# Performance work log

Measured on AMD Instinct MI355X. Metric: run time of the kernel, lower is better.

Reference implementation:

```python
import jax, jax.numpy as jnp
import numpy as np

D = 64          # embed_dim == latent dim
T = 200         # diffusion_steps, timestep_respacing='' -> full 200 reverse steps
B, L = 8192, 100
N_ITEMS = 100000


def setup_inputs() -> dict:
    key = jax.random.key(0)
    ks = jax.random.split(key, 16)

    def lin(k, i, o):
        return (jax.random.normal(k, (i, o), jnp.float32) / np.sqrt(i)).astype(jnp.float32)

    item_seq = jax.random.randint(ks[0], (B, L), 0, N_ITEMS)
    item_emb = jax.random.normal(ks[1], (N_ITEMS, D), jnp.float32) * 0.02
    item_emb = item_emb.at[0].set(0.0)  # padding_idx=0
    return {
        'item_seq': item_seq,
        'item_emb': item_emb,
        'W_enc1': lin(ks[2], D, 256), 'b_enc1': jnp.zeros((256,), jnp.float32),
        'W_enc2': lin(ks[3], 256, 2 * D), 'b_enc2': jnp.zeros((2 * D,), jnp.float32),
        'W_in': lin(ks[4], D, D), 'b_in': jnp.zeros((D,), jnp.float32),
        'W_t': lin(ks[5], D, D), 'b_t': jnp.zeros((D,), jnp.float32),
        'W_c': lin(ks[6], D, D), 'b_c': jnp.zeros((D,), jnp.float32),
        'W_out': lin(ks[7], D, D), 'b_out': jnp.zeros((D,), jnp.float32),
    }


def _schedule():
    # improved-diffusion linear schedule
    scale = 1000.0 / T
    betas = jnp.linspace(scale * 1e-4, scale * 0.02, T, dtype=jnp.float32)
    alphas = 1.0 - betas
    acp = jnp.cumprod(alphas)
    acp_prev = jnp.concatenate([jnp.ones((1,), jnp.float32), acp[:-1]])
    sqrt_recip = jnp.sqrt(1.0 / acp)
    sqrt_recipm1 = jnp.sqrt(1.0 / acp - 1.0)
    post_var = betas * (1.0 - acp_prev) / (1.0 - acp)
    post_logvar = jnp.log(jnp.concatenate([post_var[1:2], post_var[1:]]))  # clipped
    coef1 = betas * jnp.sqrt(acp_prev) / (1.0 - acp)
    coef2 = (1.0 - acp_prev) * jnp.sqrt(alphas) / (1.0 - acp)
    return sqrt_recip, sqrt_recipm1, post_logvar, coef1, coef2


def reference(item_seq, item_emb, W_enc1, b_enc1, W_enc2, b_enc2,
              W_in, b_in, W_t, b_t, W_c, b_c, W_out, b_out):
    # ---- pooled VAE encoder (eval mode: dropout = identity, z = mu) ----
    seq = item_emb[item_seq]                                   # [B, L, D] gather
    cnt = jnp.sum(item_seq != 0, axis=1, keepdims=True).astype(seq.dtype)
    pooled = jnp.sum(seq, axis=1) / jnp.sqrt(cnt)              # [B, D]
    h = jax.nn.relu(pooled @ W_enc1 + b_enc1)
    enc = h @ W_enc2 + b_enc2                                  # [B, 2D]
    mu, logvar = jnp.split(enc, 2, axis=-1)
    z = mu                                                     # eval reparameterize

    # ---- ScoreNet: eps-prediction MLP conditioned on x_start and sinusoidal t ----
    half = D // 2
    freqs = jnp.exp(-jnp.log(10000.0) * jnp.arange(half, dtype=jnp.float32) / half)

    def scorenet(x, t_float, cond):
        ang = t_float * freqs                                  # [D/2]
        temb = jnp.concatenate([jnp.cos(ang), jnp.sin(ang)])   # [D]
        hh = jax.nn.silu(x @ W_in + b_in + (temb @ W_t + b_t) + cond @ W_c + b_c)
        return hh @ W_out + b_out                              # eps, [B, D]

    # ---- p_sample_loop (FIXED_SMALL variance, clip_denoised=True) ----
    sqrt_recip, sqrt_recipm1, post_logvar, coef1, coef2 = _schedule()
    x_init = jax.random.normal(jax.random.key(1), z.shape, z.dtype)
    noise_key = jax.random.key(2)

    def step(x, t):
        eps = scorenet(x, t.astype(jnp.float32), z)
        x0 = jnp.clip(sqrt_recip[t] * x - sqrt_recipm1[t] * eps, -1.0, 1.0)
        mean = coef1[t] * x0 + coef2[t] * x
        noise = jax.random.normal(jax.random.fold_in(noise_key, t), x.shape, x.dtype)
        sigma = jnp.where(t > 0, jnp.exp(0.5 * post_logvar[t]), 0.0)
        return mean + sigma * noise, None

    sample, _ = jax.lax.scan(step, x_init, jnp.arange(T - 1, -1, -1))
    return sample
```

## Files before the change

### kernel.cpp

```cpp
#include <hip/hip_runtime.h>
#include <cstdint>


#define DEVI __device__ __forceinline__

typedef __attribute__((ext_vector_type(8))) short short8;
typedef __attribute__((ext_vector_type(4))) float f32x4;

DEVI void threefry2x32(uint32_t k0, uint32_t k1, uint32_t x0, uint32_t x1,
                       uint32_t &o0, uint32_t &o1)
{
  const uint32_t ks2 = k0 ^ k1 ^ 0x1BD11BDAu;
  x0 += k0; x1 += k1;
#define TFR(r) { x0 += x1; x1 = __builtin_rotateleft32(x1, r); x1 ^= x0; }
  TFR(13u) TFR(15u) TFR(26u) TFR(6u)   x0 += k1;  x1 += ks2 + 1u;
  TFR(17u) TFR(29u) TFR(16u) TFR(24u)  x0 += ks2; x1 += k0 + 2u;
  TFR(13u) TFR(15u) TFR(26u) TFR(6u)   x0 += k0;  x1 += k1 + 3u;
  TFR(17u) TFR(29u) TFR(16u) TFR(24u)  x0 += k1;  x1 += ks2 + 4u;
  TFR(13u) TFR(15u) TFR(26u) TFR(6u)   x0 += ks2; x1 += k0 + 5u;
#undef TFR
  o0 = x0; o1 = x1;
}

DEVI uint32_t jax_random_bits32(uint32_t k0, uint32_t k1, uint32_t j)
{
  uint32_t a, b;
  threefry2x32(k0, k1, 0u, j, a, b);
  return a ^ b;
}

DEVI float jax_bits_to_normal(uint32_t bits)
{
  const float LO = -0.99999994f;
  float f = __uint_as_float((bits >> 9) | 0x3f800000u) - 1.0f;
  float u = fmaxf(LO, f * 2.0f + LO);
  float w = -__logf((1.0f - u) * (1.0f + u));
  float p;
  if (w < 5.0f) {
    w = w - 2.5f;
    p =              2.81022636e-08f;
    p = fmaf(p, w,   3.43273939e-07f);
    p = fmaf(p, w,  -3.5233877e-06f);
    p = fmaf(p, w,  -4.39150654e-06f);
    p = fmaf(p, w,   0.00021858087f);
    p = fmaf(p, w,  -0.00125372503f);
    p = fmaf(p, w,  -0.00417768164f);
    p = fmaf(p, w,   0.246640727f);
    p = fmaf(p, w,   1.50140941f);
  } else {
    w = sqrtf(w) - 3.0f;
    p =             -0.000200214257f;
    p = fmaf(p, w,   0.000100950558f);
    p = fmaf(p, w,   0.00134934322f);
    p = fmaf(p, w,  -0.00367342844f);
    p = fmaf(p, w,   0.00573950773f);
    p = fmaf(p, w,  -0.0076224613f);
    p = fmaf(p, w,   0.00943887047f);
    p = fmaf(p, w,   1.00167406f);
    p = fmaf(p, w,   2.83297682f);
  }
  return 1.41421356237f * (p * u);
}

DEVI short bf16_hi_trunc(float x) { return (short)(__float_as_uint(x) >> 16); }
DEVI float bf16_to_f32(short h)
{
  return __uint_as_float(((uint32_t)(unsigned short)h) << 16);
}
DEVI void split_bf16(float x, short &h, short &l)
{
  h = bf16_hi_trunc(x);
  float r = x - bf16_to_f32(h);
  l = bf16_hi_trunc(r);
}

DEVI short8 ld_frag16(const short* p)
{
  union { int4 v; short8 s; } u;
  u.v = *(const int4*)p;
  return u.s;
}

__global__ __launch_bounds__(64)
void k_prep(const float* __restrict__ Wt, const float* __restrict__ bt,
            const float* __restrict__ bin, float* __restrict__ tpb,
            float* __restrict__ sched)
{
  __shared__ float temb[64];
  const int t = blockIdx.x;
  const int d = threadIdx.x;
  const float lg = logf(10000.0f);
  {
    int i = d & 31;
    float fr  = expf((-lg * (float)i) / 32.0f);
    float ang = (float)t * fr;
    temb[d] = (d < 32) ? cosf(ang) : sinf(ang);
  }
  if (d == 0) {
    const float start = (float)(5.0 * 1e-4);
    const float stop  = (float)(5.0 * 0.02);
    const float delta = stop - start;
    float prod = 1.f, acp_prev = 1.f, beta = 0.f, alpha = 1.f;
    for (int i = 0; i <= t; ++i) {
      beta  = start + ((float)i * delta) / 199.0f;
      alpha = 1.0f - beta;
      acp_prev = prod;
      prod = prod * alpha;
    }
    float acp = prod;
    float om  = 1.0f - acp;
    sched[t * 8 + 0] = sqrtf(1.0f / acp);
    sched[t * 8 + 1] = sqrtf(1.0f / acp - 1.0f);
    sched[t * 8 + 2] = beta * sqrtf(acp_prev) / om;
    sched[t * 8 + 3] = (1.0f - acp_prev) * sqrtf(alpha) / om;
    float pv = beta * (1.0f - acp_prev) / om;
    sched[t * 8 + 4] = (t > 0) ? sqrtf(pv) : 0.0f;
    uint32_t fk0, fk1;
    threefry2x32(0u, 2u, 0u, (uint32_t)t, fk0, fk1);
    ((uint32_t*)sched)[t * 8 + 5] = fk0;
    ((uint32_t*)sched)[t * 8 + 6] = fk1;
  }
  __syncthreads();
  float acc = bt[d] + bin[d];
  for (int k = 0; k < 64; ++k)
    acc = fmaf(temb[k], Wt[k * 64 + d], acc);
  tpb[t * 64 + d] = acc;
}

#define XLDW  72
#define NBW   68

__global__
__attribute__((amdgpu_flat_work_group_size(512, 512), amdgpu_waves_per_eu(4, 4)))
void k_ddpm(const int* __restrict__ seq, const float* __restrict__ emb,
            const float* __restrict__ W1, const float* __restrict__ b1,
            const float* __restrict__ W2, const float* __restrict__ b2,
            const float* __restrict__ Wc, const float* __restrict__ bc,
            const float* __restrict__ Win, const float* __restrict__ Wout,
            const float* __restrict__ bout,
            const float* __restrict__ tpb, const float* __restrict__ sched,
            float* __restrict__ out)
{
  __shared__ __align__(16) char smem[28672];

  const int tid  = threadIdx.x;
  const int lane = tid & 63;
  const int w    = tid >> 6;
  const bool gemv = (w < 4);
  const int r0g  = blockIdx.x * 16;
  const uint32_t* su = (const uint32_t*)sched;

  const int nt   = w & 3;
  const int nn   = lane & 15;
  const int quad = lane >> 4;
  const int dim  = nt * 16 + nn;
  const int arow = nn;
  const int kq0  = quad * 8;
  const int kq1  = 32 + quad * 8;
  const int rowb = quad * 4;

  const int cb   = w * 128 + lane * 2;
  const uint32_t jn = (uint32_t)(r0g * 64 + cb);
  const int nrow = cb >> 6;
  const int ndim = cb & 63;

  {
    float* pool_s = (float*)smem;
    float* h_s    = (float*)(smem + 4096);
    float* mu_s   = (float*)(smem + 20480);
    float* cp_s   = (float*)(smem + 24576);

#pragma unroll
    for (int i = 0; i < 2; ++i) {
      int c = tid + i * 512;
      int row = c >> 6, d = c & 63;
      const int* rowp = seq + (r0g + row) * 100;
      float s = 0.f; int cnt = 0;
      for (int l = 0; l < 100; ++l) {
        int id = rowp[l];
        cnt += (id != 0);
        s += emb[id * 64 + d];
      }
      pool_s[row * 64 + d] = s / sqrtf((float)cnt);
    }
    __syncthreads();

#pragma unroll
    for (int i = 0; i < 8; ++i) {
      int c = tid + i * 512;
      int row = c >> 8, j = c & 255;
      float a = b1[j];
      for (int k = 0; k < 64; ++k)
        a = fmaf(pool_s[row * 64 + k], W1[k * 256 + j], a);
      h_s[row * 256 + j] = fmaxf(a, 0.f);
    }
    __syncthreads();

#pragma unroll
    for (int i = 0; i < 2; ++i) {
      int c = tid + i * 512;
      int row = c >> 6, j = c & 63;
      float a = b2[j];
      for (int k = 0; k < 256; ++k)
        a = fmaf(h_s[row * 256 + k], W2[k * 128 + j], a);
      mu_s[row * 64 + j] = a;
    }
    __syncthreads();

#pragma unroll
    for (int i = 0; i < 2; ++i) {
      int c = tid + i * 512;
      int row = c >> 6, j = c & 63;
      float a = bc[j];
      for (int k = 0; k < 64; ++k)
        a = fmaf(mu_s[row * 64 + k], Wc[k * 64 + j], a);
      cp_s[row * 64 + j] = a;
    }
    __syncthreads();
  }

  float cp[4] = {0.f, 0.f, 0.f, 0.f};
  if (gemv) {
    const float* cp_s = (const float*)(smem + 24576);
#pragma unroll
    for (int r = 0; r < 4; ++r) cp[r] = cp_s[(rowb + r) * 64 + dim];
  }
  __syncthreads();

  short* Xh = (short*)smem;
  short* Xl = (short*)(smem + 2304);
  short* Hh = (short*)(smem + 4608);
  short* Hl = (short*)(smem + 6912);
  float* nbuf = (float*)(smem + 9216);
  float* nb_w = &nbuf[nrow * NBW + ndim];

  short8 wiH0, wiL0, wiH1, wiL1, woH0, woL0, woH1, woL1;
  float xo[4] = {0.f, 0.f, 0.f, 0.f};
  float bo = 0.f, tp = 0.f;
  uint32_t j0 = 0;

  if (gemv) {
#pragma unroll
    for (int j = 0; j < 8; ++j) {
      short h, l;
      split_bf16(Win[(kq0 + j) * 64 + dim], h, l);  wiH0[j] = h; wiL0[j] = l;
      split_bf16(Win[(kq1 + j) * 64 + dim], h, l);  wiH1[j] = h; wiL1[j] = l;
      split_bf16(Wout[(kq0 + j) * 64 + dim], h, l); woH0[j] = h; woL0[j] = l;
      split_bf16(Wout[(kq1 + j) * 64 + dim], h, l); woH1[j] = h; woL1[j] = l;
    }
    bo = bout[dim];
    j0 = (uint32_t)((r0g + rowb) * 64 + dim);
#pragma unroll
    for (int r = 0; r < 4; ++r) {
      xo[r] = jax_bits_to_normal(jax_random_bits32(0u, 1u, j0 + r * 64u));
      short h, l;
      split_bf16(xo[r], h, l);
      Xh[(rowb + r) * XLDW + dim] = h; Xl[(rowb + r) * XLDW + dim] = l;
    }
    tp = tpb[199 * 64 + dim];
  }
  {
    const uint32_t fk0 = su[199 * 8 + 5];
    const uint32_t fk1 = su[199 * 8 + 6];
    float* d = nb_w + 16 * NBW;
    d[0] = jax_bits_to_normal(jax_random_bits32(fk0, fk1, jn + 0u));
    d[1] = jax_bits_to_normal(jax_random_bits32(fk0, fk1, jn + 1u));
  }
  __syncthreads();

#pragma unroll 1
  for (int t = 199; t >= 0; --t) {
    uint32_t gk0 = 0, gk1 = 0;
    float* nd = nullptr;
    if (t > 0) {
      gk0 = su[(t - 1) * 8 + 5];
      gk1 = su[(t - 1) * 8 + 6];
      nd = nb_w + ((t - 1) & 1) * 16 * NBW;
    }

    float sr = 0.f, srm1 = 0.f, c1 = 0.f, c2 = 0.f, sg = 0.f, tpn = 0.f;
    f32x4 acc;

    if (gemv) {
      sr   = sched[t * 8 + 0];
      srm1 = sched[t * 8 + 1];
      c1   = sched[t * 8 + 2];
      c2   = sched[t * 8 + 3];
      sg   = sched[t * 8 + 4];

#pragma unroll
      for (int r = 0; r < 4; ++r) acc[r] = tp + cp[r];
      {
        short8 xh0 = ld_frag16(&Xh[arow * XLDW + kq0]);
        short8 xl0 = ld_frag16(&Xl[arow * XLDW + kq0]);
        short8 xh1 = ld_frag16(&Xh[arow * XLDW + kq1]);
        short8 xl1 = ld_frag16(&Xl[arow * XLDW + kq1]);
        acc = __builtin_amdgcn_mfma_f32_16x16x32_bf16(xl0, wiH0, acc, 0, 0, 0);
        acc = __builtin_amdgcn_mfma_f32_16x16x32_bf16(xh0, wiL0, acc, 0, 0, 0);
        acc = __builtin_amdgcn_mfma_f32_16x16x32_bf16(xh0, wiH0, acc, 0, 0, 0);
        acc = __builtin_amdgcn_mfma_f32_16x16x32_bf16(xl1, wiH1, acc, 0, 0, 0);
        acc = __builtin_amdgcn_mfma_f32_16x16x32_bf16(xh1, wiL1, acc, 0, 0, 0);
        acc = __builtin_amdgcn_mfma_f32_16x16x32_bf16(xh1, wiH1, acc, 0, 0, 0);
      }
#pragma unroll
      for (int r = 0; r < 4; ++r) {
        float v = acc[r];
        v = v * __builtin_amdgcn_rcpf(1.0f + __expf(-v));
        short h, l;
        split_bf16(v, h, l);
        Hh[(rowb + r) * XLDW + dim] = h; Hl[(rowb + r) * XLDW + dim] = l;
      }
      int tn = (t > 0) ? (t - 1) : 0;
      tpn = tpb[tn * 64 + dim];
    }
    uint32_t b0 = 0, b1v = 0;
    if (t > 0) {
      b0  = jax_random_bits32(gk0, gk1, jn + 0u);
      b1v = jax_random_bits32(gk0, gk1, jn + 1u);
    }
    __syncthreads();

    if (gemv) {
      float n[4];
      const float* nr = &nbuf[(t & 1) * 16 * NBW + rowb * NBW + dim];
#pragma unroll
      for (int r = 0; r < 4; ++r) n[r] = nr[r * NBW];

      f32x4 eac;
#pragma unroll
      for (int r = 0; r < 4; ++r) eac[r] = bo;
      {
        short8 hh0 = ld_frag16(&Hh[arow * XLDW + kq0]);
        short8 hl0 = ld_frag16(&Hl[arow * XLDW + kq0]);
        short8 hh1 = ld_frag16(&Hh[arow * XLDW + kq1]);
        short8 hl1 = ld_frag16(&Hl[arow * XLDW + kq1]);
        eac = __builtin_amdgcn_mfma_f32_16x16x32_bf16(hl0, woH0, eac, 0, 0, 0);
        eac = __builtin_amdgcn_mfma_f32_16x16x32_bf16(hh0, woL0, eac, 0, 0, 0);
        eac = __builtin_amdgcn_mfma_f32_16x16x32_bf16(hh0, woH0, eac, 0, 0, 0);
        eac = __builtin_amdgcn_mfma_f32_16x16x32_bf16(hl1, woH1, eac, 0, 0, 0);
        eac = __builtin_amdgcn_mfma_f32_16x16x32_bf16(hh1, woL1, eac, 0, 0, 0);
        eac = __builtin_amdgcn_mfma_f32_16x16x32_bf16(hh1, woH1, eac, 0, 0, 0);
      }
#pragma unroll
      for (int r = 0; r < 4; ++r) {
        float xc = fminf(1.f, fmaxf(-1.f, sr * xo[r] - srm1 * eac[r]));
        xo[r] = c1 * xc + c2 * xo[r] + sg * n[r];
        short h, l;
        split_bf16(xo[r], h, l);
        Xh[(rowb + r) * XLDW + dim] = h; Xl[(rowb + r) * XLDW + dim] = l;
      }
      tp = tpn;
    }
    if (t > 0) {
      nd[0] = jax_bits_to_normal(b0);
      nd[1] = jax_bits_to_normal(b1v);
    }
    __syncthreads();
  }

  if (gemv) {
#pragma unroll
    for (int r = 0; r < 4; ++r) out[j0 + r * 64u] = xo[r];
  }
}

extern "C" void kernel_launch(void* const* d_in, const int* in_sizes, int n_in,
                              void* d_out, int out_size, void* d_ws, size_t ws_size,
                              hipStream_t stream)
{
  const int*   seq  = (const int*)  d_in[0];
  const float* emb  = (const float*)d_in[1];
  const float* W1   = (const float*)d_in[2];
  const float* b1   = (const float*)d_in[3];
  const float* W2   = (const float*)d_in[4];
  const float* b2   = (const float*)d_in[5];
  const float* Win  = (const float*)d_in[6];
  const float* bin  = (const float*)d_in[7];
  const float* Wt   = (const float*)d_in[8];
  const float* bt   = (const float*)d_in[9];
  const float* Wc   = (const float*)d_in[10];
  const float* bc   = (const float*)d_in[11];
  const float* Wout = (const float*)d_in[12];
  const float* bout = (const float*)d_in[13];

  float* out   = (float*)d_out;
  float* ws    = (float*)d_ws;
  float* tpb   = ws;
  float* sched = ws + 12800;

  k_prep <<<200, 64, 0, stream>>>(Wt, bt, bin, tpb, sched);
  k_ddpm <<<512, 512, 0, stream>>>(seq, emb, W1, b1, W2, b2, Wc, bc,
                                   Win, Wout, bout, tpb, sched, out);
}
```

Measured before the change: 560.8 us.

## Split pooling encoder into separate high-parallelism kernel merged with schedule prep

Moves the embedding gather, pooling, encoder MLP and condition projection out of the 512-block diffusion kernel into a new kernel with 1024 blocks of 256 threads, which also handles the per-timestep schedule and time-embedding work in 200 extra blocks. The condition projection goes to a workspace buffer that the diffusion kernel reads back per thread. The aim is to spread the memory-bound gather across more blocks and occupancy than the 512-thread kernel with its fixed waves-per-EU allowed, and to shrink that kernel's shared memory. The cost is a round trip through global memory for the projected condition.

Result: faster. 547.8 us (-2.3%).

```diff
diff --git a/kernel.cpp b/kernel.cpp
--- a/kernel.cpp
+++ b/kernel.cpp
@@ -81,50 +81,113 @@
   return u.s;
 }
 
-__global__ __launch_bounds__(64)
-void k_prep(const float* __restrict__ Wt, const float* __restrict__ bt,
-            const float* __restrict__ bin, float* __restrict__ tpb,
-            float* __restrict__ sched)
-{
-  __shared__ float temb[64];
-  const int t = blockIdx.x;
-  const int d = threadIdx.x;
-  const float lg = logf(10000.0f);
-  {
-    int i = d & 31;
-    float fr  = expf((-lg * (float)i) / 32.0f);
-    float ang = (float)t * fr;
-    temb[d] = (d < 32) ? cosf(ang) : sinf(ang);
-  }
-  if (d == 0) {
-    const float start = (float)(5.0 * 1e-4);
-    const float stop  = (float)(5.0 * 0.02);
-    const float delta = stop - start;
-    float prod = 1.f, acp_prev = 1.f, beta = 0.f, alpha = 1.f;
-    for (int i = 0; i <= t; ++i) {
-      beta  = start + ((float)i * delta) / 199.0f;
-      alpha = 1.0f - beta;
-      acp_prev = prod;
-      prod = prod * alpha;
-    }
-    float acp = prod;
-    float om  = 1.0f - acp;
-    sched[t * 8 + 0] = sqrtf(1.0f / acp);
-    sched[t * 8 + 1] = sqrtf(1.0f / acp - 1.0f);
-    sched[t * 8 + 2] = beta * sqrtf(acp_prev) / om;
-    sched[t * 8 + 3] = (1.0f - acp_prev) * sqrtf(alpha) / om;
-    float pv = beta * (1.0f - acp_prev) / om;
-    sched[t * 8 + 4] = (t > 0) ? sqrtf(pv) : 0.0f;
-    uint32_t fk0, fk1;
-    threefry2x32(0u, 2u, 0u, (uint32_t)t, fk0, fk1);
-    ((uint32_t*)sched)[t * 8 + 5] = fk0;
-    ((uint32_t*)sched)[t * 8 + 6] = fk1;
-  }
-  __syncthreads();
-  float acc = bt[d] + bin[d];
-  for (int k = 0; k < 64; ++k)
-    acc = fmaf(temb[k], Wt[k * 64 + d], acc);
-  tpb[t * 64 + d] = acc;
+__global__ __launch_bounds__(256)
+void k_poolenc(const int* __restrict__ seq, const float* __restrict__ emb,
+               const float* __restrict__ W1, const float* __restrict__ b1,
+               const float* __restrict__ W2, const float* __restrict__ b2,
+               const float* __restrict__ Wc, const float* __restrict__ bc,
+               float* __restrict__ cproj,
+               const float* __restrict__ Wt, const float* __restrict__ bt,
+               const float* __restrict__ bin, float* __restrict__ tpb,
+               float* __restrict__ sched)
+{
+  __shared__ float p_s[8 * 64];
+  __shared__ float h_s[8 * 256];
+  __shared__ float mu_s[8 * 64];
+  const int tid = threadIdx.x;
+
+  if (blockIdx.x < 1024u) {
+    const int r0 = blockIdx.x * 8;
+
+#pragma unroll
+    for (int i = 0; i < 2; ++i) {
+      int c = tid + i * 256;
+      int row = c >> 6, d = c & 63;
+      const int* rowp = seq + (r0 + row) * 100;
+      float s = 0.f; int cnt = 0;
+      for (int l = 0; l < 100; ++l) {
+        int id = rowp[l];
+        cnt += (id != 0);
+        s += emb[id * 64 + d];
+      }
+      p_s[row * 64 + d] = s / sqrtf((float)cnt);
+    }
+    __syncthreads();
+
+#pragma unroll
+    for (int i = 0; i < 8; ++i) {
+      int c = tid + i * 256;
+      int row = c >> 8, j = c & 255;
+      float a = b1[j];
+      for (int k = 0; k < 64; ++k)
+        a = fmaf(p_s[row * 64 + k], W1[k * 256 + j], a);
+      h_s[row * 256 + j] = fmaxf(a, 0.f);
+    }
+    __syncthreads();
+
+#pragma unroll
+    for (int i = 0; i < 2; ++i) {
+      int c = tid + i * 256;
+      int row = c >> 6, j = c & 63;
+      float a = b2[j];
+      for (int k = 0; k < 256; ++k)
+        a = fmaf(h_s[row * 256 + k], W2[k * 128 + j], a);
+      mu_s[row * 64 + j] = a;
+    }
+    __syncthreads();
+
+#pragma unroll
+    for (int i = 0; i < 2; ++i) {
+      int c = tid + i * 256;
+      int row = c >> 6, j = c & 63;
+      float a = bc[j];
+      for (int k = 0; k < 64; ++k)
+        a = fmaf(mu_s[row * 64 + k], Wc[k * 64 + j], a);
+      cproj[(r0 + row) * 64 + j] = a;
+    }
+  } else {
+    __shared__ float temb[64];
+    const int t = blockIdx.x - 1024;
+    const int d = tid;
+    if (d < 64) {
+      const float lg = logf(10000.0f);
+      int i = d & 31;
+      float fr  = expf((-lg * (float)i) / 32.0f);
+      float ang = (float)t * fr;
+      temb[d] = (d < 32) ? cosf(ang) : sinf(ang);
+      if (d == 0) {
+        const float start = (float)(5.0 * 1e-4);
+        const float stop  = (float)(5.0 * 0.02);
+        const float delta = stop - start;
+        float prod = 1.f, acp_prev = 1.f, beta = 0.f, alpha = 1.f;
+        for (int i2 = 0; i2 <= t; ++i2) {
+          beta  = start + ((float)i2 * delta) / 199.0f;
+          alpha = 1.0f - beta;
+          acp_prev = prod;
+          prod = prod * alpha;
+        }
+        float acp = prod;
+        float om  = 1.0f - acp;
+        sched[t * 8 + 0] = sqrtf(1.0f / acp);
+        sched[t * 8 + 1] = sqrtf(1.0f / acp - 1.0f);
+        sched[t * 8 + 2] = beta * sqrtf(acp_prev) / om;
+        sched[t * 8 + 3] = (1.0f - acp_prev) * sqrtf(alpha) / om;
+        float pv = beta * (1.0f - acp_prev) / om;
+        sched[t * 8 + 4] = (t > 0) ? sqrtf(pv) : 0.0f;
+        uint32_t fk0, fk1;
+        threefry2x32(0u, 2u, 0u, (uint32_t)t, fk0, fk1);
+        ((uint32_t*)sched)[t * 8 + 5] = fk0;
+        ((uint32_t*)sched)[t * 8 + 6] = fk1;
+      }
+    }
+    __syncthreads();
+    if (d < 64) {
+      float acc = bt[d] + bin[d];
+      for (int k = 0; k < 64; ++k)
+        acc = fmaf(temb[k], Wt[k * 64 + d], acc);
+      tpb[t * 64 + d] = acc;
+    }
+  }
 }
 
 #define XLDW  72
@@ -132,16 +195,14 @@
 
 __global__
 __attribute__((amdgpu_flat_work_group_size(512, 512), amdgpu_waves_per_eu(4, 4)))
-void k_ddpm(const int* __restrict__ seq, const float* __restrict__ emb,
-            const float* __restrict__ W1, const float* __restrict__ b1,
-            const float* __restrict__ W2, const float* __restrict__ b2,
-            const float* __restrict__ Wc, const float* __restrict__ bc,
-            const float* __restrict__ Win, const float* __restrict__ Wout,
+void k_ddpm(const float* __restrict__ Win, const float* __restrict__ Wout,
             const float* __restrict__ bout,
-            const float* __restrict__ tpb, const float* __restrict__ sched,
-            float* __restrict__ out)
-{
-  __shared__ __align__(16) char smem[28672];
+            const float* __restrict__ cproj, const float* __restrict__ tpb,
+            const float* __restrict__ sched, float* __restrict__ out)
+{
+  __shared__ __align__(16) short Xh[16 * XLDW], Xl[16 * XLDW];
+  __shared__ __align__(16) short Hh[16 * XLDW], Hl[16 * XLDW];
+  __shared__ __align__(16) float nbuf[2 * 16 * NBW];
 
   const int tid  = threadIdx.x;
   const int lane = tid & 63;
@@ -163,79 +224,10 @@
   const uint32_t jn = (uint32_t)(r0g * 64 + cb);
   const int nrow = cb >> 6;
   const int ndim = cb & 63;
-
-  {
-    float* pool_s = (float*)smem;
-    float* h_s    = (float*)(smem + 4096);
-    float* mu_s   = (float*)(smem + 20480);
-    float* cp_s   = (float*)(smem + 24576);
-
-#pragma unroll
-    for (int i = 0; i < 2; ++i) {
-      int c = tid + i * 512;
-      int row = c >> 6, d = c & 63;
-      const int* rowp = seq + (r0g + row) * 100;
-      float s = 0.f; int cnt = 0;
-      for (int l = 0; l < 100; ++l) {
-        int id = rowp[l];
-        cnt += (id != 0);
-        s += emb[id * 64 + d];
-      }
-      pool_s[row * 64 + d] = s / sqrtf((float)cnt);
-    }
-    __syncthreads();
-
-#pragma unroll
-    for (int i = 0; i < 8; ++i) {
-      int c = tid + i * 512;
-      int row = c >> 8, j = c & 255;
-      float a = b1[j];
-      for (int k = 0; k < 64; ++k)
-        a = fmaf(pool_s[row * 64 + k], W1[k * 256 + j], a);
-      h_s[row * 256 + j] = fmaxf(a, 0.f);
-    }
-    __syncthreads();
-
-#pragma unroll
-    for (int i = 0; i < 2; ++i) {
-      int c = tid + i * 512;
-      int row = c >> 6, j = c & 63;
-      float a = b2[j];
-      for (int k = 0; k < 256; ++k)
-        a = fmaf(h_s[row * 256 + k], W2[k * 128 + j], a);
-      mu_s[row * 64 + j] = a;
-    }
-    __syncthreads();
-
-#pragma unroll
-    for (int i = 0; i < 2; ++i) {
-      int c = tid + i * 512;
-      int row = c >> 6, j = c & 63;
-      float a = bc[j];
-      for (int k = 0; k < 64; ++k)
-        a = fmaf(mu_s[row * 64 + k], Wc[k * 64 + j], a);
-      cp_s[row * 64 + j] = a;
-    }
-    __syncthreads();
-  }
-
-  float cp[4] = {0.f, 0.f, 0.f, 0.f};
-  if (gemv) {
-    const float* cp_s = (const float*)(smem + 24576);
-#pragma unroll
-    for (int r = 0; r < 4; ++r) cp[r] = cp_s[(rowb + r) * 64 + dim];
-  }
-  __syncthreads();
-
-  short* Xh = (short*)smem;
-  short* Xl = (short*)(smem + 2304);
-  short* Hh = (short*)(smem + 4608);
-  short* Hl = (short*)(smem + 6912);
-  float* nbuf = (float*)(smem + 9216);
   float* nb_w = &nbuf[nrow * NBW + ndim];
 
   short8 wiH0, wiL0, wiH1, wiL1, woH0, woL0, woH1, woL1;
-  float xo[4] = {0.f, 0.f, 0.f, 0.f};
+  float cp[4] = {0.f, 0.f, 0.f, 0.f}, xo[4] = {0.f, 0.f, 0.f, 0.f};
   float bo = 0.f, tp = 0.f;
   uint32_t j0 = 0;
 
@@ -250,6 +242,8 @@
     }
     bo = bout[dim];
     j0 = (uint32_t)((r0g + rowb) * 64 + dim);
+#pragma unroll
+    for (int r = 0; r < 4; ++r) cp[r] = cproj[j0 + r * 64u];
 #pragma unroll
     for (int r = 0; r < 4; ++r) {
       xo[r] = jax_bits_to_normal(jax_random_bits32(0u, 1u, j0 + r * 64u));
@@ -385,10 +379,11 @@
 
   float* out   = (float*)d_out;
   float* ws    = (float*)d_ws;
-  float* tpb   = ws;
-  float* sched = ws + 12800;
-
-  k_prep <<<200, 64, 0, stream>>>(Wt, bt, bin, tpb, sched);
-  k_ddpm <<<512, 512, 0, stream>>>(seq, emb, W1, b1, W2, b2, Wc, bc,
-                                   Win, Wout, bout, tpb, sched, out);
-}
+  float* cproj = ws;
+  float* tpb   = ws + 524288;
+  float* sched = ws + 524288 + 12800;
+
+  k_poolenc<<<1224, 256, 0, stream>>>(seq, emb, W1, b1, W2, b2, Wc, bc,
+                                      cproj, Wt, bt, bin, tpb, sched);
+  k_ddpm <<<512, 512, 0, stream>>>(Win, Wout, bout, cproj, tpb, sched, out);
+}
```
